# Kernel optimization log

Hardware: AMD Instinct MI355X
Metric: run time of the kernel (lower is better)

The kernel has to match this reference:

```python
import math
import jax, jax.numpy as jnp
import numpy as np
from jax import lax

B, C, O, K, WDIM, H, W = 8, 512, 512, 3, 512, 64, 64
CONV_SCALE = 1.0 / math.sqrt(C * K * K)
MOD_SCALE = 1.0 / math.sqrt(WDIM)


def setup_inputs() -> dict:
    key = jax.random.key(0)
    k1, k2, k3, k4 = jax.random.split(key, 4)
    return {
        "x": jax.random.normal(k1, (B, C, H, W), dtype=jnp.float32),
        "w": jax.random.normal(k2, (B, WDIM), dtype=jnp.float32),
        "base_weight": jax.random.normal(k3, (1, O, C, K, K), dtype=jnp.float32),
        "mod_weight": jax.random.normal(k4, (C, WDIM), dtype=jnp.float32),
        "mod_bias": jnp.zeros((C,), dtype=jnp.float32),
    }


def reference(x, w, base_weight, mod_weight, mod_bias):
    # EqualLinear modulation: s in (B, C), then +1
    s = w @ (mod_weight * MOD_SCALE).T + mod_bias + 1.0  # (B, C)
    # Per-sample modulated weights: (B, O, C, K, K)
    weight = CONV_SCALE * base_weight * s[:, None, :, None, None]
    # Demodulation
    d = lax.rsqrt(jnp.sum(weight * weight, axis=(2, 3, 4), keepdims=True))
    weight = weight * d
    pad = K // 2

    def conv_one(xi, wi):
        # xi: (C, H, W), wi: (O, C, K, K)
        return lax.conv_general_dilated(
            xi[None], wi, window_strides=(1, 1),
            padding=[(pad, pad), (pad, pad)],
            dimension_numbers=("NCHW", "OIHW", "NCHW"),
        )[0]

    return jax.vmap(conv_one)(x, weight)  # (B, O, H, W)
```

## Files before the change

### kernel.cpp

```cpp
#include <hip/hip_runtime.h>
#include <stdint.h>


#define MOD_SCALE  0.044194173824159216f
#define CONV_SCALE 0.014731391274719739f

typedef __attribute__((ext_vector_type(4))) float f32x4;
typedef __attribute__((ext_vector_type(8))) short bf16x8;

__device__ inline unsigned short f2bf(float f) {
  uint32_t u = __float_as_uint(f);
  uint32_t r = (u + 0x7fffu + ((u >> 16) & 1u)) >> 16;
  return (unsigned short)r;
}

__device__ inline void gload_lds16(const void* g, void* l) {
  __builtin_amdgcn_global_load_lds(
      (const __attribute__((address_space(1))) void*)g,
      (__attribute__((address_space(3))) void*)l, 16, 0, 0);
}

__global__ __launch_bounds__(256) void k_style(const float* __restrict__ w,
                                               const float* __restrict__ modw,
                                               const float* __restrict__ modb,
                                               float* __restrict__ s_out) {
  __shared__ float red[256];
  const int tid = threadIdx.x;
  const int sb = blockIdx.x;
  const int cb = sb & 7, b = sb >> 3;
  const int cl = tid >> 2, qq = tid & 3;
  const int c = (cb << 6) + cl;
  const float4* wd = (const float4*)(w + (b << 9) + (qq << 7));
  const float4* md = (const float4*)(modw + ((size_t)c << 9) + (qq << 7));
  float acc = 0.f;
#pragma unroll
  for (int i = 0; i < 32; ++i) {
    float4 a = wd[i], m = md[i];
    acc += a.x * m.x + a.y * m.y + a.z * m.z + a.w * m.w;
  }
  red[tid] = acc;
  __syncthreads();
  if (tid < 64) {
    float v = red[tid * 4] + red[tid * 4 + 1] + red[tid * 4 + 2] + red[tid * 4 + 3];
    int cc = (cb << 6) + tid;
    s_out[(b << 9) + cc] = v * MOD_SCALE + modb[cc] + 1.0f;
  }
}

__global__ __launch_bounds__(256) void k_prep(const float* __restrict__ x,
                                              const float* __restrict__ s,
                                              unsigned short* __restrict__ xp) {
  __shared__ unsigned short smem[64 * 65];
  const int blk = blockIdx.x;
  const int tid = threadIdx.x;
  if (blk < 4096) {
    const int b = blk >> 9, r = blk & 511;
    const int c0 = ((r >> 6) << 6), p0 = ((r & 63) << 6);
    {
      const int pi = tid & 63, ci0 = tid >> 6;
      const float* src = x + (size_t)((b << 9) + c0 + ci0) * 4096 + p0 + pi;
      const float* sv = s + (b << 9) + c0 + ci0;
#pragma unroll
      for (int it = 0; it < 16; ++it)
        smem[(ci0 + (it << 2)) * 65 + pi] =
            f2bf(src[(size_t)(it << 2) * 4096] * sv[it << 2]);
    }
    __syncthreads();
    {
      const int cq = tid & 31, pq = tid >> 5;
#pragma unroll
      for (int it = 0; it < 8; ++it) {
        const int p = pq + (it << 3);
        const int gp = p0 + p;
        const int py = (gp >> 6) + 1, px = (gp & 63) + 1;
        uint32_t v = (uint32_t)smem[(cq << 1) * 65 + p] |
                     ((uint32_t)smem[((cq << 1) + 1) * 65 + p] << 16);
        ((uint32_t*)(xp + ((size_t)b * 4356 + py * 66 + px) * 512 + c0))[cq] = v;
      }
    }
  } else {
    const int q = blk - 4096;
    const int b = q / 260, p = q - b * 260;
    int py, px;
    if (p < 66)       { py = 0;       px = p; }
    else if (p < 132) { py = 65;      px = p - 66; }
    else if (p < 196) { py = p - 131; px = 0; }
    else              { py = p - 195; px = 65; }
    uint32_t* dst = (uint32_t*)(xp + ((size_t)b * 4356 + py * 66 + px) * 512);
    dst[tid] = 0u;
  }
}

__global__ __launch_bounds__(256) void k_fwd(const float* __restrict__ bw,
                                             const float* __restrict__ s,
                                             unsigned short* __restrict__ awT,
                                             float* __restrict__ d_out) {
  __shared__ float lw[4608];
  __shared__ float ls[4096];
  __shared__ float red[32];
  const int tid = threadIdx.x;
  const int o = blockIdx.x;
  {
    const float4* src = (const float4*)(bw + (size_t)o * 4608);
    float4* dst = (float4*)lw;
#pragma unroll
    for (int i = 0; i < 4; ++i) dst[tid + (i << 8)] = src[tid + (i << 8)];
    if (tid < 128) dst[tid + 1024] = src[tid + 1024];
  }
  {
    const float4* src = (const float4*)s;
    float4* dst = (float4*)ls;
#pragma unroll
    for (int i = 0; i < 4; ++i) dst[tid + (i << 8)] = src[tid + (i << 8)];
  }
  __syncthreads();
  const int c0 = tid << 1;
  const int base = c0 * 9;
  float wq0 = 0.f, wq1 = 0.f;
#pragma unroll
  for (int j = 0; j < 9; ++j) {
    float a = lw[base + j];      wq0 += a * a;
    float b2 = lw[base + 9 + j]; wq1 += b2 * b2;
  }
  const int lane = tid & 63, wv = tid >> 6;
#pragma unroll
  for (int b = 0; b < 8; ++b) {
    float s0 = ls[(b << 9) + c0], s1 = ls[(b << 9) + c0 + 1];
    float v = wq0 * s0 * s0 + wq1 * s1 * s1;
#pragma unroll
    for (int off = 32; off > 0; off >>= 1) v += __shfl_down(v, off, 64);
    if (lane == 0) red[(b << 2) + wv] = v;
  }
  __syncthreads();
  if (tid < 8) {
    float a = red[tid << 2] + red[(tid << 2) + 1] + red[(tid << 2) + 2] + red[(tid << 2) + 3];
    d_out[(tid << 9) + o] = rsqrtf(a * (1.0f / 4608.0f)) * CONV_SCALE;
  }
  uint32_t* dst = (uint32_t*)(awT + (size_t)o * 4608);
#pragma unroll
  for (int j = 0; j < 9; ++j)
    dst[(j << 8) + tid] = (uint32_t)f2bf(lw[base + j]) |
                          ((uint32_t)f2bf(lw[base + 9 + j]) << 16);
}

__global__ __launch_bounds__(256, 2) void k_conv(const unsigned short* __restrict__ awT,
                                                 const unsigned short* __restrict__ xpad,
                                                 const float* __restrict__ dmod,
                                                 float* __restrict__ out) {
  __shared__ alignas(16) unsigned short As[3 * 8192];
  __shared__ alignas(16) unsigned short Bs[8448];
  const int tid = threadIdx.x;
  const int b  = blockIdx.z;
  const int m0 = blockIdx.y << 7;
  const int n0 = blockIdx.x << 7;
  const int y0 = n0 >> 6;

  const int srow = tid >> 3;
  const int schk = ((tid & 7) - (srow & 7)) & 7;
  const int scol = schk << 3;

  const unsigned short* A0 = awT + (size_t)(m0 + srow) * 4608 + scol;
  const size_t bx = (size_t)b * (66 * 66 * 512);

  const int lane = tid & 63;
  const int wv   = tid >> 6;
  const int moff = (wv >> 1) << 6;
  const int noff = (wv & 1) << 6;
  const int noffp = noff ? 66 : 0;
  const int lm   = lane & 15;
  const int g4   = lane >> 4;

  const unsigned short* ardA[2];
#pragma unroll
  for (int h = 0; h < 2; ++h)
    ardA[h] = As + (moff + lm) * 64 + ((((h << 2) + g4) + moff + lm) & 7) * 8;
  const unsigned short* ardB[3][2];
#pragma unroll
  for (int kx = 0; kx < 3; ++kx) {
    const int rb = noffp + lm + kx;
#pragma unroll
    for (int h = 0; h < 2; ++h)
      ardB[kx][h] = Bs + rb * 64 + ((((h << 2) + g4) + rb) & 7) * 8;
  }

  f32x4 acc[4][4];
#pragma unroll
  for (int i = 0; i < 4; ++i)
#pragma unroll
    for (int j = 0; j < 4; ++j) acc[i][j] = (f32x4){0.f, 0.f, 0.f, 0.f};

#pragma unroll 1
  for (int ky = 0; ky < 3; ++ky) {
    const unsigned short* Bp0 = xpad + bx + (size_t)((y0 + ky) * 66 + srow) * 512 + scol;
#pragma unroll 1
    for (int kb = 0; kb < 8; ++kb) {
      const int kcol = kb << 6;
#pragma unroll
      for (int kx = 0; kx < 3; ++kx) {
        const unsigned short* Ap = A0 + ((ky * 3 + kx) << 9) + kcol;
#pragma unroll
        for (int g = 0; g < 4; ++g)
          gload_lds16(Ap + g * (32 * 4608), As + ((kx << 13) + (((g << 8) + tid) << 3)));
      }
      const unsigned short* Bp = Bp0 + kcol;
#pragma unroll
      for (int g = 0; g < 4; ++g)
        gload_lds16(Bp + g * (32 * 512), Bs + (((g << 8) + tid) << 3));
      if (tid < 32) gload_lds16(Bp + 128 * 512, Bs + 8192 + tid * 8);
      __syncthreads();
#pragma unroll
      for (int kx = 0; kx < 3; ++kx) {
#pragma unroll
        for (int h = 0; h < 2; ++h) {
          bf16x8 af[4], bf[4];
          const unsigned short* pa = ardA[h] + (kx << 13);
          const unsigned short* pb = ardB[kx][h];
#pragma unroll
          for (int i = 0; i < 4; ++i) af[i] = *(const bf16x8*)(pa + (i << 10));
#pragma unroll
          for (int j = 0; j < 4; ++j) bf[j] = *(const bf16x8*)(pb + (j << 10));
#pragma unroll
          for (int i = 0; i < 4; ++i)
#pragma unroll
            for (int j = 0; j < 4; ++j)
              acc[i][j] = __builtin_amdgcn_mfma_f32_16x16x32_bf16(af[i], bf[j], acc[i][j], 0, 0, 0);
        }
      }
      __syncthreads();
    }
  }

  const float* dB = dmod + (b << 9) + m0 + moff;
  float* op = out + (size_t)((b << 9) + m0 + moff) * 4096 + n0 + noff;
#pragma unroll
  for (int i = 0; i < 4; ++i) {
#pragma unroll
    for (int r = 0; r < 4; ++r) {
      const int m = i * 16 + (g4 << 2) + r;
      const float dm = dB[m];
#pragma unroll
      for (int j = 0; j < 4; ++j)
        op[(size_t)m * 4096 + (j << 4) + lm] = acc[i][j][r] * dm;
    }
  }
}

extern "C" void kernel_launch(void* const* d_in, const int* in_sizes, int n_in,
                              void* d_out, int out_size, void* d_ws, size_t ws_size,
                              hipStream_t stream) {
  const float* x    = (const float*)d_in[0];
  const float* w    = (const float*)d_in[1];
  const float* bw   = (const float*)d_in[2];
  const float* modw = (const float*)d_in[3];
  const float* modb = (const float*)d_in[4];
  float* out = (float*)d_out;
  char* ws = (char*)d_ws;

  float* s_buf = (float*)(ws);
  float* d_buf = (float*)(ws + 16384);
  unsigned short* awT  = (unsigned short*)(ws + 32768);
  unsigned short* xpad = (unsigned short*)(ws + 4751360);

  (void)in_sizes; (void)n_in; (void)out_size; (void)ws_size;

  k_style<<<64,   256, 0, stream>>>(w, modw, modb, s_buf);
  k_prep <<<6176, 256, 0, stream>>>(x, s_buf, xpad);
  k_fwd  <<<512,  256, 0, stream>>>(bw, s_buf, awT, d_buf);
  k_conv <<<dim3(32, 4, 8), 256, 0, stream>>>(awT, xpad, d_buf, out);
}
```

Measured before the change: 261.5 us.

## Double-buffer LDS tiles in conv GEMM to overlap loads with MFMA

Splits the LDS tiles for A (weights) and B (padded input) into two buffers and flattens the ky/kb loops into a single 24-step pipeline. Each step issues the global-to-LDS loads for the next step before running MFMAs on the current buffer, leaving one barrier per step instead of two. LDS use roughly doubles, so launch bounds drop to one block per CU's worth of occupancy hint. This trades the latency hiding that came from two resident blocks for explicit software pipelining within one block.

```diff
diff --git a/kernel.cpp b/kernel.cpp
--- a/kernel.cpp
+++ b/kernel.cpp
@@ -143,12 +143,12 @@
                           ((uint32_t)f2bf(lw[base + 9 + j]) << 16);
 }
 
-__global__ __launch_bounds__(256, 2) void k_conv(const unsigned short* __restrict__ awT,
+__global__ __launch_bounds__(256, 1) void k_conv(const unsigned short* __restrict__ awT,
                                                  const unsigned short* __restrict__ xpad,
                                                  const float* __restrict__ dmod,
                                                  float* __restrict__ out) {
-  __shared__ alignas(16) unsigned short As[3 * 8192];
-  __shared__ alignas(16) unsigned short Bs[8448];
+  __shared__ alignas(16) unsigned short As[2][3 * 8192];
+  __shared__ alignas(16) unsigned short Bs[2][8448];
   const int tid = threadIdx.x;
   const int b  = blockIdx.z;
   const int m0 = blockIdx.y << 7;
@@ -170,17 +170,17 @@
   const int lm   = lane & 15;
   const int g4   = lane >> 4;
 
-  const unsigned short* ardA[2];
+  int aoff[2];
 #pragma unroll
   for (int h = 0; h < 2; ++h)
-    ardA[h] = As + (moff + lm) * 64 + ((((h << 2) + g4) + moff + lm) & 7) * 8;
-  const unsigned short* ardB[3][2];
+    aoff[h] = (moff + lm) * 64 + ((((h << 2) + g4) + moff + lm) & 7) * 8;
+  int boff[3][2];
 #pragma unroll
   for (int kx = 0; kx < 3; ++kx) {
     const int rb = noffp + lm + kx;
 #pragma unroll
     for (int h = 0; h < 2; ++h)
-      ardB[kx][h] = Bs + rb * 64 + ((((h << 2) + g4) + rb) & 7) * 8;
+      boff[kx][h] = rb * 64 + ((((h << 2) + g4) + rb) & 7) * 8;
   }
 
   f32x4 acc[4][4];
@@ -189,45 +189,52 @@
 #pragma unroll
     for (int j = 0; j < 4; ++j) acc[i][j] = (f32x4){0.f, 0.f, 0.f, 0.f};
 
+  auto stage = [&](int buf, int it) {
+    const int ky = it >> 3, kcol = (it & 7) << 6;
+#pragma unroll
+    for (int kx = 0; kx < 3; ++kx) {
+      const unsigned short* Ap = A0 + ((ky * 3 + kx) << 9) + kcol;
+#pragma unroll
+      for (int g = 0; g < 4; ++g)
+        gload_lds16(Ap + g * (32 * 4608),
+                    &As[buf][(kx << 13) + (((g << 8) + tid) << 3)]);
+    }
+    const unsigned short* Bp = xpad + bx + (size_t)((y0 + ky) * 66 + srow) * 512 + scol + kcol;
+#pragma unroll
+    for (int g = 0; g < 4; ++g)
+      gload_lds16(Bp + g * (32 * 512), &Bs[buf][((g << 8) + tid) << 3]);
+    if (tid < 32) gload_lds16(Bp + 128 * 512, &Bs[buf][8192 + tid * 8]);
+  };
+
+  stage(0, 0);
+  __syncthreads();
+
+  int cur = 0;
 #pragma unroll 1
-  for (int ky = 0; ky < 3; ++ky) {
-    const unsigned short* Bp0 = xpad + bx + (size_t)((y0 + ky) * 66 + srow) * 512 + scol;
-#pragma unroll 1
-    for (int kb = 0; kb < 8; ++kb) {
-      const int kcol = kb << 6;
-#pragma unroll
-      for (int kx = 0; kx < 3; ++kx) {
-        const unsigned short* Ap = A0 + ((ky * 3 + kx) << 9) + kcol;
-#pragma unroll
-        for (int g = 0; g < 4; ++g)
-          gload_lds16(Ap + g * (32 * 4608), As + ((kx << 13) + (((g << 8) + tid) << 3)));
+  for (int it = 0; it < 24; ++it) {
+    if (it < 23) stage(cur ^ 1, it + 1);
+    const unsigned short* Ab = As[cur];
+    const unsigned short* Bb = Bs[cur];
+#pragma unroll
+    for (int kx = 0; kx < 3; ++kx) {
+#pragma unroll
+      for (int h = 0; h < 2; ++h) {
+        bf16x8 af[4], bf[4];
+        const unsigned short* pa = Ab + aoff[h] + (kx << 13);
+        const unsigned short* pb = Bb + boff[kx][h];
+#pragma unroll
+        for (int i = 0; i < 4; ++i) af[i] = *(const bf16x8*)(pa + (i << 10));
+#pragma unroll
+        for (int j = 0; j < 4; ++j) bf[j] = *(const bf16x8*)(pb + (j << 10));
+#pragma unroll
+        for (int i = 0; i < 4; ++i)
+#pragma unroll
+          for (int j = 0; j < 4; ++j)
+            acc[i][j] = __builtin_amdgcn_mfma_f32_16x16x32_bf16(af[i], bf[j], acc[i][j], 0, 0, 0);
       }
-      const unsigned short* Bp = Bp0 + kcol;
-#pragma unroll
-      for (int g = 0; g < 4; ++g)
-        gload_lds16(Bp + g * (32 * 512), Bs + (((g << 8) + tid) << 3));
-      if (tid < 32) gload_lds16(Bp + 128 * 512, Bs + 8192 + tid * 8);
-      __syncthreads();
-#pragma unroll
-      for (int kx = 0; kx < 3; ++kx) {
-#pragma unroll
-        for (int h = 0; h < 2; ++h) {
-          bf16x8 af[4], bf[4];
-          const unsigned short* pa = ardA[h] + (kx << 13);
-          const unsigned short* pb = ardB[kx][h];
-#pragma unroll
-          for (int i = 0; i < 4; ++i) af[i] = *(const bf16x8*)(pa + (i << 10));
-#pragma unroll
-          for (int j = 0; j < 4; ++j) bf[j] = *(const bf16x8*)(pb + (j << 10));
-#pragma unroll
-          for (int i = 0; i < 4; ++i)
-#pragma unroll
-            for (int j = 0; j < 4; ++j)
-              acc[i][j] = __builtin_amdgcn_mfma_f32_16x16x32_bf16(af[i], bf[j], acc[i][j], 0, 0, 0);
-        }
-      }
-      __syncthreads();
-    }
+    }
+    __syncthreads();
+    cur ^= 1;
   }
 
   const float* dB = dmod + (b << 9) + m0 + moff;
```

Result: slower. 324.2 us (+24.0%).
